# Kernel tuning notes

Measured on AMD Instinct MI355X. Metric: run time of the kernel, lower is better.

## Reference

```python
import jax, jax.numpy as jnp
import numpy as np

N_NODES = 100000
D = 128
N_EDGES = 1000000


def setup_inputs() -> dict:
    key = jax.random.key(0)
    k1, k2, k3 = jax.random.split(key, 3)
    z = jax.random.normal(k1, (N_NODES, D), dtype=jnp.float32)
    edge_index = jax.random.randint(k2, (2, N_EDGES), 0, N_NODES, dtype=jnp.int64)
    # Linear(2*D, 1): weight [1, 2*D], bias [1] (torch convention)
    W = jax.random.normal(k3, (1, 2 * D), dtype=jnp.float32) * (1.0 / np.sqrt(2 * D))
    b = jnp.zeros((1,), dtype=jnp.float32)
    return {"z": z, "edge_index": edge_index, "W": W, "b": b}


def reference(z, edge_index, W, b):
    src = edge_index[0]
    dst = edge_index[1]
    # cat([z[src], z[dst]]) @ W.T == z[src] @ W_src.T + z[dst] @ W_dst.T
    # (split-weight form avoids materializing the [E, 2D] concat)
    W_src = W[:, :D]  # [1, D]
    W_dst = W[:, D:]  # [1, D]
    logits = z[src] @ W_src[0] + z[dst] @ W_dst[0] + b[0]  # [E]
    return jax.nn.sigmoid(logits)
```

## Files before the change

### kernel.cpp

```cpp
#include <hip/hip_runtime.h>
#include <hip/hip_bf16.h>

#define N_NODES 100000
#define D 128
#define N_EDGES 1000000

__global__ void __launch_bounds__(256) node_scores_kernel(
    const float* __restrict__ z, const float* __restrict__ W,
    const float* __restrict__ b, float* __restrict__ s, int n_nodes) {
  int wave = (blockIdx.x * blockDim.x + threadIdx.x) >> 6;
  int lane = threadIdx.x & 63;
  int half = lane >> 5;
  int l32  = lane & 31;
  int node = wave * 2 + half;
  if (node >= n_nodes) return;

  const float4 zv = reinterpret_cast<const float4*>(z + (size_t)node * D)[l32];
  const float4 ws = reinterpret_cast<const float4*>(W)[l32];
  const float4 wd = reinterpret_cast<const float4*>(W)[32 + l32];

  float a = zv.x * ws.x + zv.y * ws.y + zv.z * ws.z + zv.w * ws.w;
  float c = zv.x * wd.x + zv.y * wd.y + zv.z * wd.z + zv.w * wd.w;

  #pragma unroll
  for (int off = 16; off >= 1; off >>= 1) {
    a += __shfl_xor(a, off, 64);
    c += __shfl_xor(c, off, 64);
  }
  if (l32 == 0) {
    s[node] = a + b[0];
    s[n_nodes + node] = c;
  }
}

__global__ void __launch_bounds__(256) edge_kernel(
    const int* __restrict__ idx, const float* __restrict__ s,
    float* __restrict__ out, int n_edges, int n_nodes) {
  int t = blockIdx.x * blockDim.x + threadIdx.x;
  if (t * 4 >= n_edges) return;
  const int4 sv = reinterpret_cast<const int4*>(idx)[t];
  const int4 dv = reinterpret_cast<const int4*>(idx + n_edges)[t];
  const float* __restrict__ sd = s + n_nodes;

  float l0 = s[sv.x] + sd[dv.x];
  float l1 = s[sv.y] + sd[dv.y];
  float l2 = s[sv.z] + sd[dv.z];
  float l3 = s[sv.w] + sd[dv.w];

  float4 o;
  o.x = 1.0f / (1.0f + __expf(-l0));
  o.y = 1.0f / (1.0f + __expf(-l1));
  o.z = 1.0f / (1.0f + __expf(-l2));
  o.w = 1.0f / (1.0f + __expf(-l3));
  reinterpret_cast<float4*>(out)[t] = o;
}

extern "C" void kernel_launch(void* const* d_in, const int* in_sizes, int n_in,
                              void* d_out, int out_size, void* d_ws, size_t ws_size,
                              hipStream_t stream) {
  const float* z   = (const float*)d_in[0];
  const int*   idx = (const int*)d_in[1];
  const float* W   = (const float*)d_in[2];
  const float* b   = (const float*)d_in[3];
  float* out = (float*)d_out;
  float* s   = (float*)d_ws;

  int blocks1 = (N_NODES + 7) / 8;
  node_scores_kernel<<<blocks1, 256, 0, stream>>>(z, W, b, s, N_NODES);

  int blocks2 = (N_EDGES / 4 + 255) / 256;
  edge_kernel<<<blocks2, 256, 0, stream>>>(idx, s, out, N_EDGES, N_NODES);
}
```

Measured before the change: 26.37 us.

## Fuse node-score and edge kernels into one cooperative kernel with grid sync

Replaces the two kernel launches with a single cooperative launch of a fixed 1024-block grid. Each block first runs a grid-stride loop computing the per-node source and destination scores, then waits on a grid-wide barrier, then computes the edge sigmoids. Edge indices are loaded before the node phase so their latency overlaps with the node work. This removes the gap between the two launches, but adds the cost of a grid-wide barrier and makes each wave handle several node pairs in sequence instead of one.

```diff
diff --git a/kernel.cpp b/kernel.cpp
--- a/kernel.cpp
+++ b/kernel.cpp
@@ -1,58 +1,69 @@
 #include <hip/hip_runtime.h>
-#include <hip/hip_bf16.h>
+#include <hip/hip_cooperative_groups.h>
+
+namespace cg = cooperative_groups;
 
 #define N_NODES 100000
 #define D 128
 #define N_EDGES 1000000
+#define NBLOCKS 1024
+#define NTHREADS 256
 
-__global__ void __launch_bounds__(256) node_scores_kernel(
-    const float* __restrict__ z, const float* __restrict__ W,
-    const float* __restrict__ b, float* __restrict__ s, int n_nodes) {
-  int wave = (blockIdx.x * blockDim.x + threadIdx.x) >> 6;
+__global__ void __launch_bounds__(256, 4) fused_kernel(
+    const float* __restrict__ z, const int* __restrict__ idx,
+    const float* __restrict__ W, const float* __restrict__ b,
+    float* __restrict__ s, float* __restrict__ out) {
+  int tid = blockIdx.x * blockDim.x + threadIdx.x;
+
+  int4 sv = make_int4(0, 0, 0, 0), dv = make_int4(0, 0, 0, 0);
+  const bool has_edges = tid < (N_EDGES / 4);
+  if (has_edges) {
+    sv = reinterpret_cast<const int4*>(idx)[tid];
+    dv = reinterpret_cast<const int4*>(idx + N_EDGES)[tid];
+  }
+
+  int wave = tid >> 6;
   int lane = threadIdx.x & 63;
   int half = lane >> 5;
   int l32  = lane & 31;
-  int node = wave * 2 + half;
-  if (node >= n_nodes) return;
-
-  const float4 zv = reinterpret_cast<const float4*>(z + (size_t)node * D)[l32];
   const float4 ws = reinterpret_cast<const float4*>(W)[l32];
   const float4 wd = reinterpret_cast<const float4*>(W)[32 + l32];
+  const float bias = b[0];
+  const int npairs = N_NODES / 2;
+  const int wstride = (NBLOCKS * NTHREADS) / 64;
 
-  float a = zv.x * ws.x + zv.y * ws.y + zv.z * ws.z + zv.w * ws.w;
-  float c = zv.x * wd.x + zv.y * wd.y + zv.z * wd.z + zv.w * wd.w;
+  for (int p = wave; p < npairs; p += wstride) {
+    int node = p * 2 + half;
+    const float4 zv =
+        reinterpret_cast<const float4*>(z + (size_t)node * D)[l32];
+    float a = zv.x * ws.x + zv.y * ws.y + zv.z * ws.z + zv.w * ws.w;
+    float c = zv.x * wd.x + zv.y * wd.y + zv.z * wd.z + zv.w * wd.w;
+    #pragma unroll
+    for (int off = 16; off >= 1; off >>= 1) {
+      a += __shfl_xor(a, off, 64);
+      c += __shfl_xor(c, off, 64);
+    }
+    if (l32 == 0) {
+      s[node] = a + bias;
+      s[N_NODES + node] = c;
+    }
+  }
 
-  #pragma unroll
-  for (int off = 16; off >= 1; off >>= 1) {
-    a += __shfl_xor(a, off, 64);
-    c += __shfl_xor(c, off, 64);
+  cg::this_grid().sync();
+
+  if (has_edges) {
+    const float* __restrict__ sd = s + N_NODES;
+    float l0 = s[sv.x] + sd[dv.x];
+    float l1 = s[sv.y] + sd[dv.y];
+    float l2 = s[sv.z] + sd[dv.z];
+    float l3 = s[sv.w] + sd[dv.w];
+    float4 o;
+    o.x = 1.0f / (1.0f + __expf(-l0));
+    o.y = 1.0f / (1.0f + __expf(-l1));
+    o.z = 1.0f / (1.0f + __expf(-l2));
+    o.w = 1.0f / (1.0f + __expf(-l3));
+    reinterpret_cast<float4*>(out)[tid] = o;
   }
-  if (l32 == 0) {
-    s[node] = a + b[0];
-    s[n_nodes + node] = c;
-  }
-}
-
-__global__ void __launch_bounds__(256) edge_kernel(
-    const int* __restrict__ idx, const float* __restrict__ s,
-    float* __restrict__ out, int n_edges, int n_nodes) {
-  int t = blockIdx.x * blockDim.x + threadIdx.x;
-  if (t * 4 >= n_edges) return;
-  const int4 sv = reinterpret_cast<const int4*>(idx)[t];
-  const int4 dv = reinterpret_cast<const int4*>(idx + n_edges)[t];
-  const float* __restrict__ sd = s + n_nodes;
-
-  float l0 = s[sv.x] + sd[dv.x];
-  float l1 = s[sv.y] + sd[dv.y];
-  float l2 = s[sv.z] + sd[dv.z];
-  float l3 = s[sv.w] + sd[dv.w];
-
-  float4 o;
-  o.x = 1.0f / (1.0f + __expf(-l0));
-  o.y = 1.0f / (1.0f + __expf(-l1));
-  o.z = 1.0f / (1.0f + __expf(-l2));
-  o.w = 1.0f / (1.0f + __expf(-l3));
-  reinterpret_cast<float4*>(out)[t] = o;
 }
 
 extern "C" void kernel_launch(void* const* d_in, const int* in_sizes, int n_in,
@@ -65,9 +76,8 @@
   float* out = (float*)d_out;
   float* s   = (float*)d_ws;
 
-  int blocks1 = (N_NODES + 7) / 8;
-  node_scores_kernel<<<blocks1, 256, 0, stream>>>(z, W, b, s, N_NODES);
-
-  int blocks2 = (N_EDGES / 4 + 255) / 256;
-  edge_kernel<<<blocks2, 256, 0, stream>>>(idx, s, out, N_EDGES, N_NODES);
+  void* args[] = {(void*)&z, (void*)&idx, (void*)&W, (void*)&b,
+                  (void*)&s, (void*)&out};
+  hipLaunchCooperativeKernel((void*)fused_kernel, dim3(NBLOCKS),
+                             dim3(NTHREADS), args, 0, stream);
 }
```

New measurement: 103.1 us. +290.9%, slower.
